# Kernel tuning notes

Measured on AMD Instinct MI355X. Metric: run time of the kernel, lower is better.

## Reference

```python
import jax, jax.numpy as jnp
import numpy as np

B, S, C, H = 2, 2048, 1280, 20
D = C // H  # head_dim = 64


def setup_inputs() -> dict:
    key = jax.random.key(0)
    ks = jax.random.split(key, 5)
    scale = 1.0 / np.sqrt(C)
    return {
        "hidden_states": jax.random.normal(ks[0], (B, S, C), dtype=jnp.float32),
        "Wq": jax.random.normal(ks[1], (C, C), dtype=jnp.float32) * scale,
        "Wk": jax.random.normal(ks[2], (C, C), dtype=jnp.float32) * scale,
        "Wv": jax.random.normal(ks[3], (C, C), dtype=jnp.float32) * scale,
        "Wo": jax.random.normal(ks[4], (C, C), dtype=jnp.float32) * scale,
        "bo": jnp.zeros((C,), dtype=jnp.float32),
    }


def reference(hidden_states, Wq, Wk, Wv, Wo, bo):
    residual = hidden_states
    # q/k/v projections (self-attention: encoder_hidden_states is None)
    q = hidden_states @ Wq  # [B,S,C]
    k = hidden_states @ Wk
    v = hidden_states @ Wv
    # split heads -> [B,H,S,D]
    q = q.reshape(B, S, H, D).transpose(0, 2, 1, 3)
    k = k.reshape(B, S, H, D).transpose(0, 2, 1, 3)
    v = v.reshape(B, S, H, D).transpose(0, 2, 1, 3)
    scale = 1.0 / np.sqrt(D)
    scores = jnp.einsum('bhqd,bhkd->bhqk', q, k) * scale  # [B,H,S,S]
    attn_probs = jax.nn.softmax(scores, axis=-1)
    # loss term: Frobenius norm of the full attention-prob tensor (fp32)
    loss = jnp.sqrt(jnp.sum(jnp.square(attn_probs.astype(jnp.float32))))
    out = jnp.einsum('bhqk,bhkd->bhqd', attn_probs, v)  # [B,H,S,D]
    out = out.transpose(0, 2, 1, 3).reshape(B, S, C)
    out = out @ Wo + bo
    out = out + residual  # residual_connection=True, rescale_output_factor=1.0
    return out, loss
```

## Files before the change

### kernel.cpp

```cpp
#include <hip/hip_runtime.h>
#include <hip/hip_bf16.h>
#include <math.h>

#define B_SZ   2
#define S_LEN  2048
#define C_DIM  1280
#define H_NUM  20
#define D_HEAD 64
#define M_TOT  (B_SZ * S_LEN)

typedef __bf16 bf16;
typedef __bf16 bf16x8 __attribute__((ext_vector_type(8)));
typedef __bf16 bf16x4 __attribute__((ext_vector_type(4)));
typedef float  f32x4  __attribute__((ext_vector_type(4)));

__device__ inline f32x4 zero4() { f32x4 z; z[0]=z[1]=z[2]=z[3]=0.f; return z; }

__device__ __forceinline__ void async_copy16(void* lds, const void* g) {
    __builtin_amdgcn_global_load_lds(
        (const __attribute__((address_space(1))) unsigned int*)g,
        (__attribute__((address_space(3))) unsigned int*)lds,
        16, 0, 0);
}

__global__ __launch_bounds__(256) void k_prep(
    const float* __restrict__ hs, bf16* __restrict__ hs_bf,
    const float* __restrict__ w0, const float* __restrict__ w1,
    const float* __restrict__ w2, const float* __restrict__ w3,
    bf16* __restrict__ o0, bf16* __restrict__ o1,
    bf16* __restrict__ o2, bf16* __restrict__ o3) {
    if (blockIdx.x < 5120) {
        int i = (blockIdx.x * 256 + threadIdx.x) * 4;
        float4 v = *(const float4*)(hs + i);
        bf16x4 o; o[0]=(bf16)v.x; o[1]=(bf16)v.y; o[2]=(bf16)v.z; o[3]=(bf16)v.w;
        *(bf16x4*)(hs_bf + i) = o;
        return;
    }
    __shared__ float t[32][33];
    int idx = blockIdx.x - 5120;
    int zi  = idx / 1600;
    int rem = idx % 1600;
    int k0 = (rem / 40) * 32, n0 = (rem % 40) * 32;
    const float* w = zi==0 ? w0 : zi==1 ? w1 : zi==2 ? w2 : w3;
    bf16*       o  = zi==0 ? o0 : zi==1 ? o1 : zi==2 ? o2 : o3;
    int tx = threadIdx.x & 31, ty = threadIdx.x >> 5;
    #pragma unroll
    for (int i = 0; i < 32; i += 8)
        t[ty+i][tx] = w[(size_t)(k0+ty+i)*C_DIM + n0 + tx];
    __syncthreads();
    #pragma unroll
    for (int i = 0; i < 32; i += 8)
        o[(size_t)(n0+ty+i)*C_DIM + k0 + tx] = (bf16)t[tx][ty+i];
}

#define QBM 256
#define QBN 256
#define QBK 32
#define QNT (C_DIM / QBK)
__global__ __launch_bounds__(512, 2) void k_gemm_qkv(
    const bf16* __restrict__ A,
    const bf16* __restrict__ Wcat,
    bf16* __restrict__ Qo, bf16* __restrict__ Ko, bf16* __restrict__ VTo) {
    __shared__ bf16 lds[3][2][QBM][QBK];
    const int m0  = blockIdx.y * QBM;
    const int nx  = blockIdx.x;
    const int z   = nx / 5;
    const int nw0 = (nx % 5) * QBN;
    const int ng0 = nx * QBN;
    const int tid = threadIdx.x, lane = tid & 63, wid = tid >> 6;
    const int wm = wid >> 2, wn = wid & 3;
    const int g = lane >> 4, lr = lane & 15;
    const float scale = (z==0) ? 0.18033688011112042f : 1.0f;

    f32x4 acc[8][4];
    #pragma unroll
    for (int i=0;i<8;i++)
        #pragma unroll
        for (int j=0;j<4;j++)
            acc[i][j] = zero4();

#define QSTAGE(bf, kt)                                                       \
    { const int k0_ = (kt)*QBK;                                              \
      _Pragma("unroll")                                                      \
      for (int c = 0; c < 2; ++c) {                                          \
        int p = c*512 + tid;                                                 \
        int row = p >> 2, gp = p & 3;                                        \
        async_copy16((char*)&lds[bf][0][0][0] + p*16,                        \
                     &A[(size_t)(m0+row)*C_DIM + k0_ + gp*8]);               \
        async_copy16((char*)&lds[bf][1][0][0] + p*16,                        \
                     &Wcat[(size_t)(ng0+row)*C_DIM + k0_ + gp*8]);           \
      } }

    QSTAGE(0, 0);
    QSTAGE(1, 1);
    asm volatile("s_waitcnt vmcnt(4)" ::: "memory");
    __builtin_amdgcn_s_barrier();

    int cur = 0;
    for (int t = 0; t < QNT; ++t) {
        if (t + 2 < QNT) {
            int sb = cur + 2; if (sb >= 3) sb -= 3;
            QSTAGE(sb, t + 2);
        }
        const bf16* AB = &lds[cur][0][0][0];
        const bf16* BB = &lds[cur][1][0][0];
        bf16x8 af[8], bfr[4];
        #pragma unroll
        for (int mf = 0; mf < 8; ++mf)
            af[mf] = *(const bf16x8*)(AB + (wm*128 + mf*16 + lr)*QBK + g*8);
        #pragma unroll
        for (int nf = 0; nf < 4; ++nf)
            bfr[nf] = *(const bf16x8*)(BB + (wn*64 + nf*16 + lr)*QBK + g*8);
        #pragma unroll
        for (int mf = 0; mf < 8; ++mf)
            #pragma unroll
            for (int nf = 0; nf < 4; ++nf)
                acc[mf][nf] = __builtin_amdgcn_mfma_f32_16x16x32_bf16(
                    af[mf], bfr[nf], acc[mf][nf], 0,0,0);
        if (t + 2 < QNT) asm volatile("s_waitcnt vmcnt(4) lgkmcnt(0)" ::: "memory");
        else             asm volatile("s_waitcnt vmcnt(0) lgkmcnt(0)" ::: "memory");
        __builtin_amdgcn_s_barrier();
        if (++cur == 3) cur = 0;
    }

    if (z == 2) {
        #pragma unroll
        for (int mf=0;mf<8;mf++) {
            #pragma unroll
            for (int nf=0;nf<4;nf++) {
                int n = nw0 + wn*64 + nf*16 + lr;
                int h = n >> 6, d = n & 63;
                int m = m0 + wm*128 + mf*16 + g*4;
                int b = m >> 11, s = m & (S_LEN-1);
                bf16x4 ov;
                #pragma unroll
                for (int r=0;r<4;r++) ov[r] = (bf16)acc[mf][nf][r];
                *(bf16x4*)&VTo[((size_t)(b*H_NUM + h)*D_HEAD + d)*S_LEN + s] = ov;
            }
        }
    } else {
        bf16* Out = (z==0) ? Qo : Ko;
        #pragma unroll
        for (int mf=0;mf<8;mf++) {
            #pragma unroll
            for (int nf=0;nf<4;nf++) {
                int n = nw0 + wn*64 + nf*16 + lr;
                int h = n >> 6, d = n & 63;
                #pragma unroll
                for (int r=0;r<4;r++) {
                    int m = m0 + wm*128 + mf*16 + g*4 + r;
                    int b = m >> 11, s = m & (S_LEN-1);
                    Out[(size_t)((b*H_NUM + h)*S_LEN + s)*D_HEAD + d] = (bf16)(acc[mf][nf][r] * scale);
                }
            }
        }
    }
}

#define BM 128
#define BN 128
#define BK 64

#define GEMM_STAGE(Al, Bl, Aptr, Bptr, m0, n0, k0)                                \
    {                                                                             \
        _Pragma("unroll")                                                         \
        for (int c = 0; c < 4; ++c) {                                             \
            int p = c*256 + tid;                                                  \
            int row = p >> 3, gp = p & 7, gc = gp ^ (row & 7);                    \
            async_copy16((char*)(Al) + p*16,                                      \
                         &Aptr[(size_t)((m0)+row)*C_DIM + (k0) + gc*8]);          \
            async_copy16((char*)(Bl) + p*16,                                      \
                         &Bptr[(size_t)((n0)+row)*C_DIM + (k0) + gc*8]);          \
        }                                                                         \
    }

#define GEMM_COMPUTE(Al, Bl)                                                      \
    {                                                                             \
        _Pragma("unroll")                                                         \
        for (int kk = 0; kk < 2; ++kk) {                                          \
            bf16x8 af[4], bfr[4];                                                 \
            _Pragma("unroll")                                                     \
            for (int mf = 0; mf < 4; ++mf) {                                      \
                int arow = wm*64 + mf*16 + lr;                                    \
                af[mf] = *(const bf16x8*)((char*)(Al) + arow*128 +                \
                          (((kk*4 + g) ^ (arow & 7)) << 4));                      \
            }                                                                     \
            _Pragma("unroll")                                                     \
            for (int nf = 0; nf < 4; ++nf) {                                      \
                int brow = wn*64 + nf*16 + lr;                                    \
                bfr[nf] = *(const bf16x8*)((char*)(Bl) + brow*128 +               \
                          (((kk*4 + g) ^ (brow & 7)) << 4));                      \
            }                                                                     \
            _Pragma("unroll")                                                     \
            for (int mf = 0; mf < 4; ++mf)                                        \
                _Pragma("unroll")                                                 \
                for (int nf = 0; nf < 4; ++nf)                                    \
                    acc[mf][nf] = __builtin_amdgcn_mfma_f32_16x16x32_bf16(        \
                        af[mf], bfr[nf], acc[mf][nf], 0,0,0);                     \
        }                                                                         \
    }

__global__ __launch_bounds__(256) void k_gemm_out(
    const bf16* __restrict__ A,
    const bf16* __restrict__ WoT,
    const float* __restrict__ bo,
    const float* __restrict__ res,
    float* __restrict__ out,
    const float* __restrict__ lossPart, int nLoss) {
    __shared__ bf16 Al[2][BM][BK];
    __shared__ bf16 Bl[2][BN][BK];
    __shared__ float wred[4];
    const int m0 = blockIdx.y * BM, n0 = blockIdx.x * BN;
    const int tid = threadIdx.x, lane = tid & 63, wid = tid >> 6;
    const int wm = wid >> 1, wn = wid & 1;
    const int g = lane >> 4, lr = lane & 15;
    f32x4 acc[4][4];
    #pragma unroll
    for (int i=0;i<4;i++)
        #pragma unroll
        for (int j=0;j<4;j++)
            acc[i][j] = zero4();
    GEMM_STAGE(&Al[0][0][0], &Bl[0][0][0], A, WoT, m0, n0, 0);
    asm volatile("s_waitcnt vmcnt(0)" ::: "memory");
    __builtin_amdgcn_s_barrier();
    int cur = 0;
    for (int k0 = 0; k0 < C_DIM; k0 += BK) {
        if (k0 + BK < C_DIM)
            GEMM_STAGE(&Al[cur^1][0][0], &Bl[cur^1][0][0], A, WoT, m0, n0, k0 + BK);
        GEMM_COMPUTE(&Al[cur][0][0], &Bl[cur][0][0]);
        asm volatile("s_waitcnt vmcnt(0) lgkmcnt(0)" ::: "memory");
        __builtin_amdgcn_s_barrier();
        cur ^= 1;
    }
    #pragma unroll
    for (int mf=0;mf<4;mf++) {
        #pragma unroll
        for (int nf=0;nf<4;nf++) {
            int n = n0 + wn*64 + nf*16 + lr;
            float bias = bo[n];
            #pragma unroll
            for (int r=0;r<4;r++) {
                int m = m0 + wm*64 + mf*16 + g*4 + r;
                size_t idx = (size_t)m*C_DIM + n;
                out[idx] = acc[mf][nf][r] + bias + res[idx];
            }
        }
    }
    if (blockIdx.x == 0 && blockIdx.y == 0) {
        float s = 0.f;
        for (int i = tid; i < nLoss; i += 256) s += lossPart[i];
        #pragma unroll
        for (int msk=1; msk<64; msk<<=1) s += __shfl_xor(s, msk);
        if (lane == 0) wred[wid] = s;
        __syncthreads();
        if (tid == 0) out[(size_t)M_TOT*C_DIM] = sqrtf(wred[0]+wred[1]+wred[2]+wred[3]);
    }
}

#define KVB 64
#define NT_ (S_LEN / KVB)
__global__ __launch_bounds__(512) void k_attn(
    const bf16* __restrict__ Q,
    const bf16* __restrict__ Kg,
    const bf16* __restrict__ VT,
    bf16* __restrict__ O,
    float* __restrict__ lossPart) {
    __shared__ bf16 Kl[3][KVB][64];
    __shared__ bf16 Vl[3][D_HEAD][64];

    const int id  = blockIdx.x;
    const int fid = (id & 7) * 40 + (id >> 3);
    const int bh = fid >> 3;
    const int qb = fid & 7;
    const int b = bh / H_NUM, hh = bh % H_NUM;
    const int tid = threadIdx.x, lane = tid & 63, wid = tid >> 6;
    const int g = lane >> 4, lr = lane & 15;

    const bf16* Kbase = Kg + (size_t)bh * S_LEN * D_HEAD;
    const bf16* Vbase = VT + (size_t)bh * D_HEAD * S_LEN;

    bf16x8 aq[2][2];
    int qrow[2];
    #pragma unroll
    for (int h=0; h<2; ++h) {
        qrow[h] = qb*256 + wid*32 + h*16 + lr;
        const bf16* qp = Q + ((size_t)bh*S_LEN + qrow[h])*D_HEAD;
        aq[h][0] = *(const bf16x8*)(qp + g*8);
        aq[h][1] = *(const bf16x8*)(qp + 32 + g*8);
    }

    bf16x8 ones;
    #pragma unroll
    for (int i=0;i<8;i++) ones[i] = (bf16)1.0f;

    const int lb7 = (lr & 3) | (((lr >> 2) & 1) << 2);
    const int lhi = ((lr >> 2) & 2) << 3;

    f32x4 o_acc[2][4];
    f32x4 l_acc[2], s2m[2];
    #pragma unroll
    for (int h=0;h<2;++h) {
        #pragma unroll
        for (int i=0;i<4;i++) o_acc[h][i] = zero4();
        l_acc[h] = zero4(); s2m[h] = zero4();
    }

#define STAGE(buf, kv0)                                                          \
    {                                                                            \
        {                                                                        \
            int p = tid;                                                         \
            int lrow = p >> 3, gp = p & 7;                                       \
            int tl = (lrow & 51) | ((lrow & 4) << 1) | ((lrow & 8) >> 1);        \
            async_copy16((char*)&Kl[buf][0][0] + p*16,                           \
                         Kbase + (size_t)((kv0) + tl)*D_HEAD                     \
                               + ((gp ^ (lrow & 7)) << 3));                      \
        }                                                                        \
        {                                                                        \
            int p = tid;                                                         \
            int drow = p >> 3, gp = p & 7;                                       \
            async_copy16((char*)&Vl[buf][0][0] + p*16,                           \
                         Vbase + (size_t)drow*S_LEN + (kv0)                      \
                               + ((gp ^ (drow & 7)) << 3));                      \
        }                                                                        \
    }

    STAGE(0, 0);
    STAGE(1, KVB);
    asm volatile("s_waitcnt vmcnt(2)" ::: "memory");
    __builtin_amdgcn_s_barrier();

    int cur = 0;
    for (int t = 0; t < NT_; ++t) {
        if (t + 2 < NT_) {
            int sb = cur + 2; if (sb >= 3) sb -= 3;
            STAGE(sb, (t+2)*KVB);
        }
        const bf16* KB = &Kl[cur][0][0];
        const bf16* VB = &Vl[cur][0][0];

        f32x4 accp[2][2][2];
        __builtin_amdgcn_s_setprio(1);
        #pragma unroll
        for (int pair=0; pair<2; ++pair)
            #pragma unroll
            for (int u=0; u<2; ++u) {
                const bf16* kr = KB + (pair*32 + (u<<3) + lhi + lb7)*64;
                bf16x8 k0 = *(const bf16x8*)(kr + ((g       ^ lb7) << 3));
                bf16x8 k1 = *(const bf16x8*)(kr + (((4 + g) ^ lb7) << 3));
                #pragma unroll
                for (int h=0; h<2; ++h) {
                    f32x4 c = zero4();
                    c = __builtin_amdgcn_mfma_f32_16x16x32_bf16(k0, aq[h][0], c, 0,0,0);
                    c = __builtin_amdgcn_mfma_f32_16x16x32_bf16(k1, aq[h][1], c, 0,0,0);
                    accp[h][pair][u] = c;
                }
            }
        __builtin_amdgcn_s_setprio(0);
        bf16x8 pb[2][2];
        #pragma unroll
        for (int h=0; h<2; ++h)
            #pragma unroll
            for (int pair=0; pair<2; ++pair)
                #pragma unroll
                for (int u=0; u<2; ++u)
                    #pragma unroll
                    for (int r=0; r<4; ++r) {
                        float e = __builtin_amdgcn_exp2f(accp[h][pair][u][r]);
                        pb[h][pair][u*4+r] = (bf16)e;
                    }
        __builtin_amdgcn_s_setprio(1);
        #pragma unroll
        for (int h=0; h<2; ++h) {
            l_acc[h] = __builtin_amdgcn_mfma_f32_16x16x32_bf16(ones, pb[h][0], l_acc[h], 0,0,0);
            l_acc[h] = __builtin_amdgcn_mfma_f32_16x16x32_bf16(ones, pb[h][1], l_acc[h], 0,0,0);
            s2m[h]   = __builtin_amdgcn_mfma_f32_16x16x32_bf16(pb[h][0], pb[h][0], s2m[h], 0,0,0);
            s2m[h]   = __builtin_amdgcn_mfma_f32_16x16x32_bf16(pb[h][1], pb[h][1], s2m[h], 0,0,0);
        }
        #pragma unroll
        for (int ds_=0; ds_<4; ++ds_) {
            const bf16* vr = VB + (ds_*16 + lr)*64;
            #pragma unroll
            for (int pair=0; pair<2; ++pair) {
                bf16x8 v = *(const bf16x8*)(vr + (((pair*4 + g) ^ (lr & 7)) << 3));
                #pragma unroll
                for (int h=0; h<2; ++h)
                    o_acc[h][ds_] = __builtin_amdgcn_mfma_f32_16x16x32_bf16(v, pb[h][pair], o_acc[h][ds_], 0,0,0);
            }
        }
        __builtin_amdgcn_s_setprio(0);
        if (t + 2 < NT_) asm volatile("s_waitcnt vmcnt(2) lgkmcnt(0)" ::: "memory");
        else             asm volatile("s_waitcnt vmcnt(0) lgkmcnt(0)" ::: "memory");
        __builtin_amdgcn_s_barrier();
        if (++cur == 3) cur = 0;
    }

    float lfull[2];
    #pragma unroll
    for (int h=0; h<2; ++h) {
        lfull[h] = l_acc[h][0];
        const float inv = 1.0f / lfull[h];
        bf16* orow = O + ((size_t)(b*S_LEN + qrow[h])*H_NUM + hh)*D_HEAD;
        #pragma unroll
        for (int ds_=0; ds_<4; ++ds_) {
            bf16x4 ov;
            #pragma unroll
            for (int r=0; r<4; ++r) ov[r] = (bf16)(o_acc[h][ds_][r] * inv);
            *(bf16x4*)(orow + ds_*16 + g*4) = ov;
        }
    }
    float v = 0.f;
    if (g == (lr >> 2)) {
        v  = s2m[0][lr & 3] / (lfull[0] * lfull[0]);
        v += s2m[1][lr & 3] / (lfull[1] * lfull[1]);
    }
    #pragma unroll
    for (int msk=1; msk<64; msk<<=1) v += __shfl_xor(v, msk);
    if (lane == 0) lossPart[(bh*8 + qb)*8 + wid] = v;
}

extern "C" void kernel_launch(void* const* d_in, const int* in_sizes, int n_in,
                              void* d_out, int out_size, void* d_ws, size_t ws_size,
                              hipStream_t stream) {
    (void)in_sizes; (void)n_in; (void)out_size; (void)ws_size;
    const float* hs = (const float*)d_in[0];
    const float* Wq = (const float*)d_in[1];
    const float* Wk = (const float*)d_in[2];
    const float* Wv = (const float*)d_in[3];
    const float* Wo = (const float*)d_in[4];
    const float* bo = (const float*)d_in[5];
    float* out = (float*)d_out;

    constexpr size_t HS_E = (size_t)M_TOT * C_DIM;
    constexpr size_t W_E  = (size_t)C_DIM * C_DIM;
    char* ws = (char*)d_ws;
    size_t off = 0;
    bf16* hs_bf = (bf16*)(ws + off); off += HS_E * 2;
    bf16* WqT   = (bf16*)(ws + off); off += W_E * 2;
    bf16* WkT   = (bf16*)(ws + off); off += W_E * 2;
    bf16* WvT   = (bf16*)(ws + off); off += W_E * 2;
    bf16* WoT   = (bf16*)(ws + off); off += W_E * 2;
    bf16* Qb    = (bf16*)(ws + off); off += HS_E * 2;
    bf16* Kb    = (bf16*)(ws + off); off += HS_E * 2;
    bf16* Vtb   = (bf16*)(ws + off); off += HS_E * 2;
    bf16* Ob    = (bf16*)(ws + off); off += HS_E * 2;
    float* lossPart = (float*)(ws + off); off += 2560 * 4;

    k_prep<<<11520, 256, 0, stream>>>(hs, hs_bf, Wq, Wk, Wv, Wo, WqT, WkT, WvT, WoT);
    k_gemm_qkv<<<dim3(3*C_DIM/QBN, M_TOT/QBM), 512, 0, stream>>>(hs_bf, WqT, Qb, Kb, Vtb);
    k_attn<<<320, 512, 0, stream>>>(Qb, Kb, Vtb, Ob, lossPart);
    k_gemm_out<<<dim3(C_DIM/BN, M_TOT/BM), 256, 0, stream>>>(Ob, WoT, bo, hs, out, lossPart, 2560);
}
```

Measured before the change: 155.3 us.

## Split attention KV range across two blocks and add combine kernel; swizzle QKV LDS

The attention kernel now splits each query block's KV sequence into two halves handled by separate blocks, doubling the grid from 320 to 640 to fill more CUs. Partial unnormalized outputs, row sums and squared sums go to workspace, and a new combine kernel merges them, normalizes, and computes per-head loss partials. The QKV GEMM also gets an XOR swizzle on its LDS layout to reduce bank conflicts on fragment loads. The split relies on the softmax having no running max, so partials can simply be added. It costs an extra kernel launch and extra global traffic, and reuses hs_bf as the second partial buffer.

```diff
diff --git a/kernel.cpp b/kernel.cpp
--- a/kernel.cpp
+++ b/kernel.cpp
@@ -84,11 +84,11 @@
       _Pragma("unroll")                                                      \
       for (int c = 0; c < 2; ++c) {                                          \
         int p = c*512 + tid;                                                 \
-        int row = p >> 2, gp = p & 3;                                        \
+        int row = p >> 2, gp = p & 3, gc = gp ^ ((row >> 1) & 3);            \
         async_copy16((char*)&lds[bf][0][0][0] + p*16,                        \
-                     &A[(size_t)(m0+row)*C_DIM + k0_ + gp*8]);               \
+                     &A[(size_t)(m0+row)*C_DIM + k0_ + gc*8]);               \
         async_copy16((char*)&lds[bf][1][0][0] + p*16,                        \
-                     &Wcat[(size_t)(ng0+row)*C_DIM + k0_ + gp*8]);           \
+                     &Wcat[(size_t)(ng0+row)*C_DIM + k0_ + gc*8]);           \
       } }
 
     QSTAGE(0, 0);
@@ -106,11 +106,15 @@
         const bf16* BB = &lds[cur][1][0][0];
         bf16x8 af[8], bfr[4];
         #pragma unroll
-        for (int mf = 0; mf < 8; ++mf)
-            af[mf] = *(const bf16x8*)(AB + (wm*128 + mf*16 + lr)*QBK + g*8);
-        #pragma unroll
-        for (int nf = 0; nf < 4; ++nf)
-            bfr[nf] = *(const bf16x8*)(BB + (wn*64 + nf*16 + lr)*QBK + g*8);
+        for (int mf = 0; mf < 8; ++mf) {
+            int arow = wm*128 + mf*16 + lr;
+            af[mf] = *(const bf16x8*)(AB + arow*QBK + ((g ^ ((arow >> 1) & 3)) << 3));
+        }
+        #pragma unroll
+        for (int nf = 0; nf < 4; ++nf) {
+            int brow = wn*64 + nf*16 + lr;
+            bfr[nf] = *(const bf16x8*)(BB + brow*QBK + ((g ^ ((brow >> 1) & 3)) << 3));
+        }
         #pragma unroll
         for (int mf = 0; mf < 8; ++mf)
             #pragma unroll
@@ -258,23 +262,28 @@
 }
 
 #define KVB 64
-#define NT_ (S_LEN / KVB)
+#define HTILES (S_LEN / KVB / 2)
 __global__ __launch_bounds__(512) void k_attn(
     const bf16* __restrict__ Q,
     const bf16* __restrict__ Kg,
     const bf16* __restrict__ VT,
-    bf16* __restrict__ O,
-    float* __restrict__ lossPart) {
+    bf16* __restrict__ O0buf,
+    bf16* __restrict__ O1buf,
+    float* __restrict__ lbuf,
+    float* __restrict__ s2buf) {
     __shared__ bf16 Kl[3][KVB][64];
     __shared__ bf16 Vl[3][D_HEAD][64];
 
     const int id  = blockIdx.x;
-    const int fid = (id & 7) * 40 + (id >> 3);
-    const int bh = fid >> 3;
-    const int qb = fid & 7;
+    const int fid = (id & 7) * 80 + (id >> 3);
+    const int bh   = fid >> 4;
+    const int rem  = fid & 15;
+    const int qb   = rem >> 1;
+    const int half = rem & 1;
     const int b = bh / H_NUM, hh = bh % H_NUM;
     const int tid = threadIdx.x, lane = tid & 63, wid = tid >> 6;
     const int g = lane >> 4, lr = lane & 15;
+    const int kvbase = half * (S_LEN/2);
 
     const bf16* Kbase = Kg + (size_t)bh * S_LEN * D_HEAD;
     const bf16* Vbase = VT + (size_t)bh * D_HEAD * S_LEN;
@@ -324,16 +333,16 @@
         }                                                                        \
     }
 
-    STAGE(0, 0);
-    STAGE(1, KVB);
+    STAGE(0, kvbase);
+    STAGE(1, kvbase + KVB);
     asm volatile("s_waitcnt vmcnt(2)" ::: "memory");
     __builtin_amdgcn_s_barrier();
 
     int cur = 0;
-    for (int t = 0; t < NT_; ++t) {
-        if (t + 2 < NT_) {
+    for (int t = 0; t < HTILES; ++t) {
+        if (t + 2 < HTILES) {
             int sb = cur + 2; if (sb >= 3) sb -= 3;
-            STAGE(sb, (t+2)*KVB);
+            STAGE(sb, kvbase + (t+2)*KVB);
         }
         const bf16* KB = &Kl[cur][0][0];
         const bf16* VB = &Vl[cur][0][0];
@@ -388,34 +397,62 @@
             }
         }
         __builtin_amdgcn_s_setprio(0);
-        if (t + 2 < NT_) asm volatile("s_waitcnt vmcnt(2) lgkmcnt(0)" ::: "memory");
-        else             asm volatile("s_waitcnt vmcnt(0) lgkmcnt(0)" ::: "memory");
+        if (t + 2 < HTILES) asm volatile("s_waitcnt vmcnt(2) lgkmcnt(0)" ::: "memory");
+        else                asm volatile("s_waitcnt vmcnt(0) lgkmcnt(0)" ::: "memory");
         __builtin_amdgcn_s_barrier();
         if (++cur == 3) cur = 0;
     }
 
-    float lfull[2];
+    bf16* Od = half ? O1buf : O0buf;
     #pragma unroll
     for (int h=0; h<2; ++h) {
-        lfull[h] = l_acc[h][0];
-        const float inv = 1.0f / lfull[h];
-        bf16* orow = O + ((size_t)(b*S_LEN + qrow[h])*H_NUM + hh)*D_HEAD;
+        bf16* orow = Od + ((size_t)(b*S_LEN + qrow[h])*H_NUM + hh)*D_HEAD;
         #pragma unroll
         for (int ds_=0; ds_<4; ++ds_) {
             bf16x4 ov;
             #pragma unroll
-            for (int r=0; r<4; ++r) ov[r] = (bf16)(o_acc[h][ds_][r] * inv);
+            for (int r=0; r<4; ++r) ov[r] = (bf16)(o_acc[h][ds_][r]);
             *(bf16x4*)(orow + ds_*16 + g*4) = ov;
         }
-    }
+        size_t base = (size_t)half*(40*2048) + (size_t)bh*2048 + qrow[h];
+        if (g == 0) lbuf[base] = l_acc[h][0];
+        if (g == (lr >> 2)) s2buf[base] = s2m[h][lr & 3];
+    }
+}
+
+__global__ __launch_bounds__(256) void k_combine(
+    bf16* __restrict__ O0, const bf16* __restrict__ O1,
+    const float* __restrict__ lbuf, const float* __restrict__ s2buf,
+    float* __restrict__ lossPart) {
+    __shared__ float wred[4];
+    const int tid = threadIdx.x, lane = tid & 63, wid = tid >> 6;
+    if (blockIdx.x < 2560) {
+        size_t e = (size_t)blockIdx.x * 2048 + (size_t)tid * 8;
+        int sg = (int)(e / C_DIM), c = (int)(e % C_DIM);
+        int b = sg >> 11, s = sg & (S_LEN-1), h = c >> 6;
+        size_t lb = (size_t)(b*H_NUM + h)*2048 + s;
+        float inv = 1.0f / (lbuf[lb] + lbuf[40*2048 + lb]);
+        bf16x8 a = *(const bf16x8*)(O0 + e);
+        bf16x8 bb = *(const bf16x8*)(O1 + e);
+        bf16x8 o;
+        #pragma unroll
+        for (int j=0;j<8;j++) o[j] = (bf16)(((float)a[j] + (float)bb[j]) * inv);
+        *(bf16x8*)(O0 + e) = o;
+        return;
+    }
+    int bh = blockIdx.x - 2560;
     float v = 0.f;
-    if (g == (lr >> 2)) {
-        v  = s2m[0][lr & 3] / (lfull[0] * lfull[0]);
-        v += s2m[1][lr & 3] / (lfull[1] * lfull[1]);
+    for (int s = tid; s < 2048; s += 256) {
+        size_t lb = (size_t)bh*2048 + s;
+        float l  = lbuf[lb]  + lbuf[40*2048 + lb];
+        float s2 = s2buf[lb] + s2buf[40*2048 + lb];
+        v += s2 / (l*l);
     }
     #pragma unroll
     for (int msk=1; msk<64; msk<<=1) v += __shfl_xor(v, msk);
-    if (lane == 0) lossPart[(bh*8 + qb)*8 + wid] = v;
+    if (lane == 0) wred[wid] = v;
+    __syncthreads();
+    if (tid == 0) lossPart[bh] = wred[0]+wred[1]+wred[2]+wred[3];
 }
 
 extern "C" void kernel_launch(void* const* d_in, const int* in_sizes, int n_in,
@@ -443,10 +480,13 @@
     bf16* Kb    = (bf16*)(ws + off); off += HS_E * 2;
     bf16* Vtb   = (bf16*)(ws + off); off += HS_E * 2;
     bf16* Ob    = (bf16*)(ws + off); off += HS_E * 2;
-    float* lossPart = (float*)(ws + off); off += 2560 * 4;
+    float* lbuf  = (float*)(ws + off); off += 2 * 40 * 2048 * 4;
+    float* s2buf = (float*)(ws + off); off += 2 * 40 * 2048 * 4;
+    float* lossPart = (float*)(ws + off); off += 40 * 4;
 
     k_prep<<<11520, 256, 0, stream>>>(hs, hs_bf, Wq, Wk, Wv, Wo, WqT, WkT, WvT, WoT);
     k_gemm_qkv<<<dim3(3*C_DIM/QBN, M_TOT/QBM), 512, 0, stream>>>(hs_bf, WqT, Qb, Kb, Vtb);
-    k_attn<<<320, 512, 0, stream>>>(Qb, Kb, Vtb, Ob, lossPart);
-    k_gemm_out<<<dim3(C_DIM/BN, M_TOT/BM), 256, 0, stream>>>(Ob, WoT, bo, hs, out, lossPart, 2560);
-}
+    k_attn<<<640, 512, 0, stream>>>(Qb, Kb, Vtb, Ob, hs_bf, lbuf, s2buf);
+    k_combine<<<2600, 256, 0, stream>>>(Ob, hs_bf, lbuf, s2buf, lossPart);
+    k_gemm_out<<<dim3(C_DIM/BN, M_TOT/BM), 256, 0, stream>>>(Ob, WoT, bo, hs, out, lossPart, 40);
+}
```

Result: no change. 157.5 us (+1.4%).
